# Optimization experiments

Hardware: AMD Instinct MI355X
Metric: run time of the kernel (lower is better)

## Reference

```python
import jax, jax.numpy as jnp
import numpy as np

B, C_IN, H_IMG, W_IMG = 64, 384, 32, 32
D, HEADS = 768, 12
HD = D // HEADS
GS = 16            # attention grid = image_size // 2
ET = 1             # extra tokens
N = GS * GS + ET   # 257
MLP_H = 4 * D
EPS = 1e-5


def _rel_index():
    coords = np.stack(np.meshgrid(np.arange(GS), np.arange(GS), indexing='ij'))  # [2,GS,GS]
    cf = coords.reshape(2, -1)                      # [2, GS*GS]
    rel = (cf[:, :, None] - cf[:, None, :]).transpose(1, 2, 0)  # [P,P,2]
    rel[:, :, 0] += GS - 1
    rel[:, :, 1] += GS - 1
    rel[:, :, 0] *= 2 * GS - 1
    idx = rel.sum(-1)                               # [P,P]
    out = np.zeros((N, N), dtype=np.int32)          # F.pad with zeros for extra tokens
    out[ET:, ET:] = idx
    return out

REL_IDX = jnp.asarray(_rel_index())


def _ln(x, g, b):
    m = x.mean(-1, keepdims=True)
    v = ((x - m) ** 2).mean(-1, keepdims=True)
    return (x - m) / jnp.sqrt(v + EPS) * g + b


def setup_inputs() -> dict:
    key = jax.random.key(0)
    ks = jax.random.split(key, 16)
    s = 0.02
    return {
        "x": jax.random.normal(ks[0], (B, C_IN, H_IMG, W_IMG), jnp.float32),
        "H": 32,
        "W": 32,
        "geo_bias": jax.random.normal(ks[1], (1, N, D), jnp.float32),
        "extra_token": jax.random.normal(ks[2], (1, ET, D), jnp.float32) * s,
        "conv_w": jax.random.normal(ks[3], (D, C_IN, 3, 3), jnp.float32) * np.sqrt(2.0 / (9 * D)),
        "conv_b": jnp.zeros((D,), jnp.float32),
        "pe_g": jnp.ones((D,), jnp.float32),
        "pe_b": jnp.zeros((D,), jnp.float32),
        "n1_g": jnp.ones((D,), jnp.float32),
        "n1_b": jnp.zeros((D,), jnp.float32),
        "qkv_w": jax.random.normal(ks[4], (3 * D, D), jnp.float32) * s,
        "rpb_table": jax.random.normal(ks[5], ((2 * GS - 1) * (2 * GS - 1), HEADS), jnp.float32) * s,
        "proj_w": jax.random.normal(ks[6], (D, D), jnp.float32) * s,
        "proj_b": jnp.zeros((D,), jnp.float32),
        "n2_g": jnp.ones((D,), jnp.float32),
        "n2_b": jnp.zeros((D,), jnp.float32),
        "fc1_w": jax.random.normal(ks[7], (MLP_H, D), jnp.float32) * s,
        "fc1_b": jnp.zeros((MLP_H,), jnp.float32),
        "fc2_w": jax.random.normal(ks[8], (D, MLP_H), jnp.float32) * s,
        "fc2_b": jnp.zeros((D,), jnp.float32),
    }


def reference(x, H, W, geo_bias, extra_token, conv_w, conv_b, pe_g, pe_b,
              n1_g, n1_b, qkv_w, rpb_table, proj_w, proj_b, n2_g, n2_b,
              fc1_w, fc1_b, fc2_w, fc2_b):
    # OverlapPatchEmbed: conv k3 s2 p1 -> [B, D, GS, GS]
    y = jax.lax.conv_general_dilated(x, conv_w, (2, 2), ((1, 1), (1, 1)),
                                     dimension_numbers=('NCHW', 'OIHW', 'NCHW'))
    y = y + conv_b[None, :, None, None]
    y = y.reshape(B, D, GS * GS).transpose(0, 2, 1)   # [B, P, D]
    y = _ln(y, pe_g, pe_b)
    tok = jnp.broadcast_to(extra_token, (B, ET, D))
    y = jnp.concatenate([tok, y], axis=1) + geo_bias  # [B, N, D]

    # Relative attention
    h = _ln(y, n1_g, n1_b)
    qkv = (h @ qkv_w.T).reshape(B, N, 3, HEADS, HD).transpose(2, 0, 3, 1, 4)
    q, k, v = qkv[0] * (HD ** -0.5), qkv[1], qkv[2]   # [B, h, N, d]
    attn = jnp.einsum('bhnd,bhmd->bhnm', q, k)
    bias = rpb_table[REL_IDX].transpose(2, 0, 1)      # [heads, N, N]
    attn = jax.nn.softmax(attn + bias[None], axis=-1)
    o = jnp.einsum('bhnm,bhmd->bhnd', attn, v).transpose(0, 2, 1, 3).reshape(B, N, D)
    y = y + (o @ proj_w.T + proj_b)

    # MLP
    h2 = _ln(y, n2_g, n2_b)
    h2 = jax.nn.gelu(h2 @ fc1_w.T + fc1_b, approximate=False)
    y = y + (h2 @ fc2_w.T + fc2_b)
    return y
```

## Files before the change

kernel.cpp:

```cpp
#include <hip/hip_runtime.h>
#include <hip/hip_bf16.h>
#include <cstdint>

using bf16 = __hip_bfloat16;
typedef __attribute__((ext_vector_type(8))) short short8;
typedef __attribute__((ext_vector_type(4))) float f32x4;


__device__ __forceinline__ void gld_lds16(const bf16* g, bf16* l) {
  __builtin_amdgcn_global_load_lds(
      (const __attribute__((address_space(1))) void*)g,
      (__attribute__((address_space(3))) void*)l, 16, 0, 0);
}

__device__ __forceinline__ unsigned short f2bf_bits(float f) {
  uint32_t u = __builtin_bit_cast(uint32_t, f);
  uint32_t r = (u + 0x7fffu + ((u >> 16) & 1u)) >> 16;
  return (unsigned short)r;
}

__device__ __forceinline__ int xcd_swz(int bid, int nwg) {
  const int q = nwg >> 3, r = nwg & 7;
  const int x = bid & 7, o = bid >> 3;
  return (x < r ? x * (q + 1) : r * (q + 1) + (x - r) * q) + o;
}

__global__ void castf2b(const float* __restrict__ in, bf16* __restrict__ out, int n) {
  int i = blockIdx.x * blockDim.x + threadIdx.x;
  int st = gridDim.x * blockDim.x;
  for (; i < n; i += st) out[i] = __float2bfloat16(in[i]);
}

__global__ void zero_b(bf16* __restrict__ p, int n) {
  int i = blockIdx.x * blockDim.x + threadIdx.x;
  if (i < n) p[i] = __float2bfloat16(0.f);
}

__global__ void convw_reorder(const float* __restrict__ w, bf16* __restrict__ o) {
  int i = blockIdx.x * blockDim.x + threadIdx.x;
  if (i >= 768 * 3456) return;
  int n = i / 3456, r = i % 3456;
  int tap = r / 384, c = r % 384;
  o[i] = __float2bfloat16(w[(long)n * 3456 + c * 9 + tap]);
}

__global__ __launch_bounds__(256, 4)
void nhwc_kernel(const float* __restrict__ x, bf16* __restrict__ xp) {
  __shared__ bf16 T[384 * 33];
  const int biy = blockIdx.x;
  const int b = biy >> 5, iy = biy & 31;
  const int tid = threadIdx.x;
  const int ix = tid & 31, cp = tid >> 5;
  const long xrow = (long)b * 384 * 1024 + iy * 32 + ix;
#pragma unroll
  for (int t = 0; t < 48; ++t) {
    const int c = t * 8 + cp;
    T[c * 33 + ix] = __float2bfloat16(x[xrow + (long)c * 1024]);
  }
  __syncthreads();
  bf16* dst = xp + (((long)b * 34 + iy + 1) * 34 + 1) * 384;
  for (int e4 = tid; e4 < 3072; e4 += 256) {
    const int e = e4 * 4;
    const int ixr = e / 384, c = e % 384;
    ushort4 v;
    v.x = ((const unsigned short*)T)[(c + 0) * 33 + ixr];
    v.y = ((const unsigned short*)T)[(c + 1) * 33 + ixr];
    v.z = ((const unsigned short*)T)[(c + 2) * 33 + ixr];
    v.w = ((const unsigned short*)T)[(c + 3) * 33 + ixr];
    *(ushort4*)(dst + e) = v;
  }
}

template <int EPI>
__global__ __launch_bounds__(256, 2)
void gemm_bt(const bf16* __restrict__ A, const bf16* __restrict__ Bw,
             const float* __restrict__ bias, float* __restrict__ outf,
             bf16* __restrict__ outb, int N, int K, int Mreal, int ntn)
{
  __shared__ bf16 As[2][128 * 64];
  __shared__ bf16 Bs[2][128 * 64];
  const int bid = xcd_swz(blockIdx.x, gridDim.x);
  const int mt = bid / ntn, nt = bid % ntn;
  const int tid = threadIdx.x;
  const int lane = tid & 63, wave = tid >> 6;
  const int wm = wave >> 1, wn = wave & 1;
  const int lr = lane & 15, lg = lane >> 4;

  f32x4 acc[4][4];
#pragma unroll
  for (int i = 0; i < 4; ++i)
#pragma unroll
    for (int j = 0; j < 4; ++j) acc[i][j] = (f32x4){0.f, 0.f, 0.f, 0.f};

  const int arow = tid >> 3;
  const int scol = (((tid & 7) ^ (arow & 7))) * 8;
  const bf16* ag = A + ((long)mt * 128 + arow) * K + scol;
  const bf16* bg = Bw + ((long)nt * 128 + arow) * K + scol;

  const int xs0 = ((lg)     ^ (lr & 7)) * 16;
  const int xs1 = ((lg + 4) ^ (lr & 7)) * 16;
  const char* pa0 = (const char*)(&As[0][0]) + (wm * 64 + lr) * 128 + xs0;
  const char* pa1 = (const char*)(&As[0][0]) + (wm * 64 + lr) * 128 + xs1;
  const char* pb0 = (const char*)(&Bs[0][0]) + (wn * 64 + lr) * 128 + xs0;
  const char* pb1 = (const char*)(&Bs[0][0]) + (wn * 64 + lr) * 128 + xs1;

  auto stage = [&](int kt, int buf) {
    const int k0 = kt << 6;
#pragma unroll
    for (int j = 0; j < 4; ++j) {
      gld_lds16(ag + (long)(j * 32) * K + k0, &As[buf][(j * 256 + tid) * 8]);
      gld_lds16(bg + (long)(j * 32) * K + k0, &Bs[buf][(j * 256 + tid) * 8]);
    }
  };
  auto compute = [&](int buf) {
    const int bo = buf * 16384;
#pragma unroll
    for (int ks = 0; ks < 2; ++ks) {
      const char* pa = ks ? pa1 : pa0;
      const char* pb = ks ? pb1 : pb0;
      short8 af[4], bv[4];
#pragma unroll
      for (int i = 0; i < 4; ++i) af[i] = *(const short8*)(pa + bo + i * 2048);
#pragma unroll
      for (int i = 0; i < 4; ++i) bv[i] = *(const short8*)(pb + bo + i * 2048);
#pragma unroll
      for (int i = 0; i < 4; ++i)
#pragma unroll
        for (int j = 0; j < 4; ++j)
          acc[i][j] = __builtin_amdgcn_mfma_f32_16x16x32_bf16(af[i], bv[j], acc[i][j], 0, 0, 0);
    }
  };

  const int nk = K >> 6;
  stage(0, 0);
  __syncthreads();
  for (int t = 0; t < nk; t += 2) {
    if (t + 1 < nk) stage(t + 1, 1);
    compute(0);
    __syncthreads();
    if (t + 1 >= nk) break;
    if (t + 2 < nk) stage(t + 2, 0);
    compute(1);
    __syncthreads();
  }

  const int rbase = mt * 128 + wm * 64 + (lane >> 4) * 4;
  const int cbase = nt * 128 + wn * 64 + lr;
#pragma unroll
  for (int i = 0; i < 4; ++i) {
#pragma unroll
    for (int j = 0; j < 4; ++j) {
      const int col = cbase + j * 16;
      float bvv = 0.f;
      if constexpr (EPI != 0) bvv = bias[col];
#pragma unroll
      for (int r = 0; r < 4; ++r) {
        const int row = rbase + i * 16 + r;
        const float v = acc[i][j][r];
        if constexpr (EPI == 0) {
          outb[(long)row * N + col] = __float2bfloat16(v);
        } else if constexpr (EPI == 1) {
          outb[(long)row * N + col] = __float2bfloat16(v + bvv);
        } else if constexpr (EPI == 2) {
          const float t = v + bvv;
          outb[(long)row * N + col] =
              __float2bfloat16(0.5f * t * (1.0f + erff(t * 0.70710678118f)));
        } else {
          if (row < Mreal) {
            const long o = (long)row * N + col;
            outf[o] = outf[o] + v + bvv;
          }
        }
      }
    }
  }
}

__global__ __launch_bounds__(256, 2)
void conv_gemm(const bf16* __restrict__ xp, const bf16* __restrict__ Bw,
               const float* __restrict__ bias, bf16* __restrict__ outb)
{
  __shared__ bf16 As[2][128 * 64];
  __shared__ bf16 Bs[2][128 * 64];
  const int bid = xcd_swz(blockIdx.x, gridDim.x);
  const int mt = bid / 6, nt = bid % 6;
  const int tid = threadIdx.x;
  const int lane = tid & 63, wave = tid >> 6;
  const int wm = wave >> 1, wn = wave & 1;
  const int lr = lane & 15, lg = lane >> 4;

  f32x4 acc[4][4];
#pragma unroll
  for (int i = 0; i < 4; ++i)
#pragma unroll
    for (int j = 0; j < 4; ++j) acc[i][j] = (f32x4){0.f, 0.f, 0.f, 0.f};

  const int arow = tid >> 3;
  const int scol = (((tid & 7) ^ (arow & 7))) * 8;
  long abase[4];
#pragma unroll
  for (int j = 0; j < 4; ++j) {
    const int m = mt * 128 + j * 32 + arow;
    const int b = m >> 8, p = m & 255;
    const int gy = p >> 4, gx = p & 15;
    abase[j] = (((long)b * 34 + 2 * gy) * 34 + 2 * gx) * 384 + scol;
  }
  const bf16* bg = Bw + ((long)nt * 128 + arow) * 3456 + scol;

  const int xs0 = ((lg)     ^ (lr & 7)) * 16;
  const int xs1 = ((lg + 4) ^ (lr & 7)) * 16;
  const char* pa0 = (const char*)(&As[0][0]) + (wm * 64 + lr) * 128 + xs0;
  const char* pa1 = (const char*)(&As[0][0]) + (wm * 64 + lr) * 128 + xs1;
  const char* pb0 = (const char*)(&Bs[0][0]) + (wn * 64 + lr) * 128 + xs0;
  const char* pb1 = (const char*)(&Bs[0][0]) + (wn * 64 + lr) * 128 + xs1;

  auto stage = [&](int kidx, int buf) {
    const int tap = kidx / 6, kc = (kidx % 6) * 64;
    const int toff = ((tap / 3) * 34 + (tap % 3)) * 384 + kc;
#pragma unroll
    for (int j = 0; j < 4; ++j) {
      gld_lds16(xp + abase[j] + toff, &As[buf][(j * 256 + tid) * 8]);
      gld_lds16(bg + (long)(j * 32) * 3456 + kidx * 64, &Bs[buf][(j * 256 + tid) * 8]);
    }
  };
  auto compute = [&](int buf) {
    const int bo = buf * 16384;
#pragma unroll
    for (int ks = 0; ks < 2; ++ks) {
      const char* pa = ks ? pa1 : pa0;
      const char* pb = ks ? pb1 : pb0;
      short8 af[4], bv[4];
#pragma unroll
      for (int i = 0; i < 4; ++i) af[i] = *(const short8*)(pa + bo + i * 2048);
#pragma unroll
      for (int i = 0; i < 4; ++i) bv[i] = *(const short8*)(pb + bo + i * 2048);
#pragma unroll
      for (int i = 0; i < 4; ++i)
#pragma unroll
        for (int j = 0; j < 4; ++j)
          acc[i][j] = __builtin_amdgcn_mfma_f32_16x16x32_bf16(af[i], bv[j], acc[i][j], 0, 0, 0);
    }
  };

  stage(0, 0);
  __syncthreads();
  for (int t = 0; t < 54; t += 2) {
    if (t + 1 < 54) stage(t + 1, 1);
    compute(0);
    __syncthreads();
    if (t + 2 < 54) stage(t + 2, 0);
    compute(1);
    __syncthreads();
  }

  const int rbase = mt * 128 + wm * 64 + (lane >> 4) * 4;
  const int cbase = nt * 128 + wn * 64 + lr;
#pragma unroll
  for (int i = 0; i < 4; ++i) {
#pragma unroll
    for (int j = 0; j < 4; ++j) {
      const int col = cbase + j * 16;
      const float bvv = bias[col];
#pragma unroll
      for (int r = 0; r < 4; ++r) {
        const int row = rbase + i * 16 + r;
        outb[(long)row * 768 + col] = __float2bfloat16(acc[i][j][r] + bvv);
      }
    }
  }
}

__global__ __launch_bounds__(256, 4)
void embed_ln_kernel(const bf16* __restrict__ CO, const float* __restrict__ extra,
                     const float* __restrict__ geo, const float* __restrict__ pe_g,
                     const float* __restrict__ pe_b, const float* __restrict__ n1_g,
                     const float* __restrict__ n1_b, float* __restrict__ y,
                     bf16* __restrict__ H)
{
  const int row = blockIdx.x;
  const int tid = threadIdx.x;
  __shared__ float red[2][4];
  const int wave = tid >> 6, lane = tid & 63;
  if (row >= 16448) {
#pragma unroll
    for (int u = 0; u < 3; ++u) H[(long)row * 768 + tid + u * 256] = __float2bfloat16(0.f);
    return;
  }
  const int b = row / 257, t = row % 257;
  float yv[3];
  if (t == 0) {
#pragma unroll
    for (int u = 0; u < 3; ++u) {
      const int d = tid + u * 256;
      yv[u] = extra[d] + geo[d];
    }
  } else {
    const bf16* src = CO + (long)(b * 256 + (t - 1)) * 768;
    float v[3]; float s = 0.f, s2 = 0.f;
#pragma unroll
    for (int u = 0; u < 3; ++u) {
      v[u] = __bfloat162float(src[tid + u * 256]);
      s += v[u]; s2 += v[u] * v[u];
    }
#pragma unroll
    for (int off = 32; off > 0; off >>= 1) { s += __shfl_xor(s, off); s2 += __shfl_xor(s2, off); }
    if (lane == 0) { red[0][wave] = s; red[1][wave] = s2; }
    __syncthreads();
    const float S = red[0][0] + red[0][1] + red[0][2] + red[0][3];
    const float S2 = red[1][0] + red[1][1] + red[1][2] + red[1][3];
    const float mean = S * (1.f / 768.f);
    const float var = S2 * (1.f / 768.f) - mean * mean;
    const float rinv = rsqrtf(var + 1e-5f);
    __syncthreads();
#pragma unroll
    for (int u = 0; u < 3; ++u) {
      const int d = tid + u * 256;
      yv[u] = (v[u] - mean) * rinv * pe_g[d] + pe_b[d] + geo[(long)t * 768 + d];
    }
  }
#pragma unroll
  for (int u = 0; u < 3; ++u) y[(long)row * 768 + tid + u * 256] = yv[u];
  float s = 0.f, s2 = 0.f;
#pragma unroll
  for (int u = 0; u < 3; ++u) { s += yv[u]; s2 += yv[u] * yv[u]; }
#pragma unroll
  for (int off = 32; off > 0; off >>= 1) { s += __shfl_xor(s, off); s2 += __shfl_xor(s2, off); }
  if (lane == 0) { red[0][wave] = s; red[1][wave] = s2; }
  __syncthreads();
  const float S = red[0][0] + red[0][1] + red[0][2] + red[0][3];
  const float S2 = red[1][0] + red[1][1] + red[1][2] + red[1][3];
  const float mean = S * (1.f / 768.f);
  const float var = S2 * (1.f / 768.f) - mean * mean;
  const float rinv = rsqrtf(var + 1e-5f);
#pragma unroll
  for (int u = 0; u < 3; ++u) {
    const int d = tid + u * 256;
    H[(long)row * 768 + d] = __float2bfloat16((yv[u] - mean) * rinv * n1_g[d] + n1_b[d]);
  }
}

__global__ __launch_bounds__(256, 4)
void ln_kernel(const float* __restrict__ y, const float* __restrict__ g,
               const float* __restrict__ bta, bf16* __restrict__ H, int Mreal)
{
  const int row = blockIdx.x;
  const int tid = threadIdx.x;
  if (row >= Mreal) {
#pragma unroll
    for (int u = 0; u < 3; ++u) H[(long)row * 768 + tid + u * 256] = __float2bfloat16(0.f);
    return;
  }
  const float* src = y + (long)row * 768;
  float v[3]; float s = 0.f, s2 = 0.f;
#pragma unroll
  for (int u = 0; u < 3; ++u) { v[u] = src[tid + u * 256]; s += v[u]; s2 += v[u] * v[u]; }
#pragma unroll
  for (int off = 32; off > 0; off >>= 1) { s += __shfl_xor(s, off); s2 += __shfl_xor(s2, off); }
  __shared__ float red[2][4];
  const int wave = tid >> 6, lane = tid & 63;
  if (lane == 0) { red[0][wave] = s; red[1][wave] = s2; }
  __syncthreads();
  const float S = red[0][0] + red[0][1] + red[0][2] + red[0][3];
  const float S2 = red[1][0] + red[1][1] + red[1][2] + red[1][3];
  const float mean = S * (1.f / 768.f);
  const float var = S2 * (1.f / 768.f) - mean * mean;
  const float rinv = rsqrtf(var + 1e-5f);
#pragma unroll
  for (int u = 0; u < 3; ++u) {
    const int d = tid + u * 256;
    H[(long)row * 768 + d] = __float2bfloat16((v[u] - mean) * rinv * g[d] + bta[d]);
  }
}

__global__ void rpbT_kernel(const float* __restrict__ rpb, float* __restrict__ rpbT) {
  int i = blockIdx.x * blockDim.x + threadIdx.x;
  if (i >= 12 * 961) return;
  int h = i / 961, t = i % 961;
  rpbT[i] = rpb[t * 12 + h];
}

__global__ __launch_bounds__(256, 2)
void vtrans_kernel(const bf16* __restrict__ qkv, bf16* __restrict__ vt) {
  __shared__ bf16 Vl[257 * 65];
  const int bh = blockIdx.x;
  const int b = bh / 12, h = bh % 12;
  const long src = (long)b * 257 * 2304 + 1536 + h * 64;
  for (int e = threadIdx.x; e < 257 * 64; e += 256) {
    const int t = e >> 6, d = e & 63;
    Vl[t * 65 + d] = qkv[src + (long)t * 2304 + d];
  }
  __syncthreads();
  const bf16 z = __float2bfloat16(0.f);
  const long dst = (long)bh * 64 * 320;
  for (int e = threadIdx.x; e < 64 * 320; e += 256) {
    const int d = e / 320, tp = e % 320;
    vt[dst + e] = (tp < 257) ? Vl[tp * 65 + d] : z;
  }
}

__global__ __launch_bounds__(256, 2)
void attn_mfma(const bf16* __restrict__ qkv, const bf16* __restrict__ vt,
               const float* __restrict__ rpbT, bf16* __restrict__ O)
{
  __shared__ bf16 Ks[64 * 64];
  __shared__ bf16 Vts[64 * 64];
  __shared__ float rpb_s[961];
  __shared__ bf16 Pl[4][16 * 72];

  const int bid = blockIdx.x;
  const int qb = bid % 5;
  const int bh = bid / 5;
  const int h = bh % 12, b = bh / 12;
  const int tid = threadIdx.x;
  const int lane = tid & 63, w = tid >> 6;
  const int lr = lane & 15, g = lane >> 4;

  for (int t = tid; t < 961; t += 256) rpb_s[t] = rpbT[h * 961 + t];

  const long qkv_bh = (long)b * 257 * 2304 + h * 64;
  const long vt_bh = (long)bh * 64 * 320;

  const int q_tok = qb * 64 + w * 16 + lr;
  const bf16* qp = qkv + qkv_bh + (long)q_tok * 2304;
  short8 qf[2];
  qf[0] = *(const short8*)(qp + g * 8);
  qf[1] = *(const short8*)(qp + 32 + g * 8);

  f32x4 ao[4];
#pragma unroll
  for (int df = 0; df < 4; ++df) ao[df] = (f32x4){0.f, 0.f, 0.f, 0.f};
  float mval = -1e30f, l = 0.f;

  for (int ck = 0; ck < 5; ++ck) {
    const int c0 = ck * 64;
#pragma unroll
    for (int it = 0; it < 2; ++it) {
      const int beta = it * 256 + tid;
      const int row = beta >> 3, cb = beta & 7;
      const int cbs = cb ^ (row & 7);
      gld_lds16(qkv + qkv_bh + (long)(c0 + row) * 2304 + 768 + cbs * 8, &Ks[beta * 8]);
      gld_lds16(vt + vt_bh + (long)row * 320 + c0 + cbs * 8, &Vts[beta * 8]);
    }
    __syncthreads();

    f32x4 st[4];
#pragma unroll
    for (int kf = 0; kf < 4; ++kf) st[kf] = (f32x4){0.f, 0.f, 0.f, 0.f};
#pragma unroll
    for (int ks = 0; ks < 2; ++ks) {
#pragma unroll
      for (int kf = 0; kf < 4; ++kf) {
        const int row = kf * 16 + lr;
        const short8 kfrag = *(const short8*)&Ks[row * 64 + ((ks * 4 + g) ^ (row & 7)) * 8];
        st[kf] = __builtin_amdgcn_mfma_f32_16x16x32_bf16(kfrag, qf[ks], st[kf], 0, 0, 0);
      }
    }

    float p[4][4];
    float t = -1e30f;
#pragma unroll
    for (int kf = 0; kf < 4; ++kf) {
#pragma unroll
      for (int r = 0; r < 4; ++r) {
        const int key = c0 + kf * 16 + g * 4 + r;
        float s;
        if (key < 257) {
          int idx = 0;
          if (q_tok > 0 && key > 0) {
            const int qi = q_tok - 1, kj = key - 1;
            idx = ((qi >> 4) - (kj >> 4) + 15) * 31 + ((qi & 15) - (kj & 15) + 15);
            idx = idx < 0 ? 0 : (idx > 960 ? 960 : idx);
          }
          s = 0.125f * st[kf][r] + rpb_s[idx];
        } else {
          s = -1e30f;
        }
        p[kf][r] = s;
        t = fmaxf(t, s);
      }
    }
    t = fmaxf(t, __shfl_xor(t, 16));
    t = fmaxf(t, __shfl_xor(t, 32));
    const float mnew = fmaxf(mval, t);
    const float corr = __expf(mval - mnew);
    mval = mnew;
    float ps = 0.f;
#pragma unroll
    for (int kf = 0; kf < 4; ++kf)
#pragma unroll
      for (int r = 0; r < 4; ++r) { p[kf][r] = __expf(p[kf][r] - mnew); ps += p[kf][r]; }
    ps += __shfl_xor(ps, 16);
    ps += __shfl_xor(ps, 32);
    l = l * corr + ps;

#pragma unroll
    for (int r = 0; r < 4; ++r) {
      const float cr = __shfl(corr, g * 4 + r);
#pragma unroll
      for (int df = 0; df < 4; ++df) ao[df][r] *= cr;
    }

    bf16* plw = &Pl[w][0];
#pragma unroll
    for (int kf = 0; kf < 4; ++kf) {
      uint2 pw;
      pw.x = ((uint32_t)f2bf_bits(p[kf][1]) << 16) | (uint32_t)f2bf_bits(p[kf][0]);
      pw.y = ((uint32_t)f2bf_bits(p[kf][3]) << 16) | (uint32_t)f2bf_bits(p[kf][2]);
      *(uint2*)&plw[lr * 72 + kf * 16 + g * 4] = pw;
    }

#pragma unroll
    for (int ks = 0; ks < 2; ++ks) {
      const short8 pa = *(const short8*)&plw[lr * 72 + ks * 32 + g * 8];
#pragma unroll
      for (int df = 0; df < 4; ++df) {
        const int row = df * 16 + lr;
        const short8 vfrag = *(const short8*)&Vts[row * 64 + ((ks * 4 + g) ^ (row & 7)) * 8];
        ao[df] = __builtin_amdgcn_mfma_f32_16x16x32_bf16(pa, vfrag, ao[df], 0, 0, 0);
      }
    }
    __syncthreads();
  }

  const float rl = 1.0f / l;
#pragma unroll
  for (int r = 0; r < 4; ++r) {
    const float rr = __shfl(rl, g * 4 + r);
    const int qg = qb * 64 + w * 16 + g * 4 + r;
    if (qg < 257) {
      bf16* op = O + ((long)b * 257 + qg) * 768 + h * 64;
#pragma unroll
      for (int df = 0; df < 4; ++df)
        op[df * 16 + lr] = __float2bfloat16(ao[df][r] * rr);
    }
  }
}


extern "C" void kernel_launch(void* const* d_in, const int* in_sizes, int n_in,
                              void* d_out, int out_size, void* d_ws, size_t ws_size,
                              hipStream_t stream) {
  (void)in_sizes; (void)n_in; (void)out_size;
  const float* x      = (const float*)d_in[0];
  const float* geo    = (const float*)d_in[3];
  const float* extra  = (const float*)d_in[4];
  const float* conv_w = (const float*)d_in[5];
  const float* conv_b = (const float*)d_in[6];
  const float* pe_g   = (const float*)d_in[7];
  const float* pe_b   = (const float*)d_in[8];
  const float* n1_g   = (const float*)d_in[9];
  const float* n1_b   = (const float*)d_in[10];
  const float* qkv_w  = (const float*)d_in[11];
  const float* rpb    = (const float*)d_in[12];
  const float* proj_w = (const float*)d_in[13];
  const float* proj_b = (const float*)d_in[14];
  const float* n2_g   = (const float*)d_in[15];
  const float* n2_b   = (const float*)d_in[16];
  const float* fc1_w  = (const float*)d_in[17];
  const float* fc1_b  = (const float*)d_in[18];
  const float* fc2_w  = (const float*)d_in[19];
  const float* fc2_b  = (const float*)d_in[20];
  float* out = (float*)d_out;

  constexpr size_t SZ_WCONV = 768UL * 3456 * 2;
  constexpr size_t SZ_WQKV  = 2304UL * 768 * 2;
  constexpr size_t SZ_WPROJ = 768UL * 768 * 2;
  constexpr size_t SZ_WFC1  = 3072UL * 768 * 2;
  constexpr size_t SZ_WFC2  = 768UL * 3072 * 2;
  constexpr size_t SZ_H     = 16512UL * 768 * 2;
  constexpr size_t SZ_A     = 16384UL * 3456 * 2;
  constexpr size_t SZ_B     = 16512UL * 768 * 2;
  constexpr size_t TOTAL = SZ_WCONV + SZ_WQKV + SZ_WPROJ + SZ_WFC1 + SZ_WFC2 + SZ_H + SZ_A + SZ_B;
  if (ws_size < TOTAL) return;

  char* ws = (char*)d_ws;
  bf16* Wconv = (bf16*)ws;                    ws += SZ_WCONV;
  bf16* Wqkv  = (bf16*)ws;                    ws += SZ_WQKV;
  bf16* Wproj = (bf16*)ws;                    ws += SZ_WPROJ;
  bf16* Wfc1  = (bf16*)ws;                    ws += SZ_WFC1;
  bf16* Wfc2  = (bf16*)ws;                    ws += SZ_WFC2;
  bf16* Hb    = (bf16*)ws;                    ws += SZ_H;
  char* regA  = ws;                           ws += SZ_A;
  char* regB  = ws;
  bf16* XP   = (bf16*)regA;
  bf16* QKV  = (bf16*)regA;
  bf16* MLPH = (bf16*)regA;
  constexpr size_t SZ_QKV = 16512UL * 2304 * 2;
  constexpr size_t SZ_XP  = 64UL * 34 * 34 * 384 * 2;
  bf16* Vt   = (bf16*)(regA + SZ_QKV);
  bf16* CO   = (bf16*)regB;
  bf16* Oat  = (bf16*)regB;
  float* rpbTp = (float*)Hb;

  convw_reorder<<<10368, 256, 0, stream>>>(conv_w, Wconv);
  castf2b<<<2048, 256, 0, stream>>>(qkv_w,  Wqkv, 1769472);
  castf2b<<<1024, 256, 0, stream>>>(proj_w, Wproj, 589824);
  castf2b<<<2048, 256, 0, stream>>>(fc1_w,  Wfc1, 2359296);
  castf2b<<<2048, 256, 0, stream>>>(fc2_w,  Wfc2, 2359296);
  hipMemsetAsync(XP, 0, SZ_XP, stream);
  nhwc_kernel<<<2048, 256, 0, stream>>>(x, XP);
  conv_gemm<<<128 * 6, 256, 0, stream>>>(XP, Wconv, conv_b, CO);
  embed_ln_kernel<<<16512, 256, 0, stream>>>(CO, extra, geo, pe_g, pe_b, n1_g, n1_b, out, Hb);
  gemm_bt<0><<<129 * 18, 256, 0, stream>>>(Hb, Wqkv, nullptr, nullptr, QKV, 2304, 768, 16448, 18);
  rpbT_kernel<<<46, 256, 0, stream>>>(rpb, rpbTp);
  vtrans_kernel<<<768, 256, 0, stream>>>(QKV, Vt);
  zero_b<<<192, 256, 0, stream>>>(Oat + 16448L * 768, 49152);
  attn_mfma<<<3840, 256, 0, stream>>>(QKV, Vt, rpbTp, Oat);
  gemm_bt<3><<<129 * 6, 256, 0, stream>>>(Oat, Wproj, proj_b, out, nullptr, 768, 768, 16448, 6);
  ln_kernel<<<16512, 256, 0, stream>>>(out, n2_g, n2_b, Hb, 16448);
  gemm_bt<2><<<129 * 24, 256, 0, stream>>>(Hb, Wfc1, fc1_b, nullptr, MLPH, 3072, 768, 16448, 24);
  gemm_bt<3><<<129 * 6, 256, 0, stream>>>(MLPH, Wfc2, fc2_b, out, nullptr, 768, 3072, 16448, 6);
}
```

Baseline: 712.1 us.

## Replace double-buffered LDS staging with single-buffer load-sync-compute loop in GEMMs

Both the generic GEMM and the conv implicit-GEMM drop their two-stage LDS ping-pong and use one buffer per operand, with a load, barrier, compute, barrier sequence each K step. This halves LDS use per block (32KB to 16KB), which could allow more resident blocks per CU. The cost is losing the overlap of global-to-LDS loads with MFMA compute inside a block, so latency has to be hidden by other resident waves instead.

```diff
diff --git a/kernel.cpp b/kernel.cpp
--- a/kernel.cpp
+++ b/kernel.cpp
@@ -77,8 +77,8 @@
              const float* __restrict__ bias, float* __restrict__ outf,
              bf16* __restrict__ outb, int N, int K, int Mreal, int ntn)
 {
-  __shared__ bf16 As[2][128 * 64];
-  __shared__ bf16 Bs[2][128 * 64];
+  __shared__ bf16 As[128 * 64];
+  __shared__ bf16 Bs[128 * 64];
   const int bid = xcd_swz(blockIdx.x, gridDim.x);
   const int mt = bid / ntn, nt = bid % ntn;
   const int tid = threadIdx.x;
@@ -99,48 +99,35 @@
 
   const int xs0 = ((lg)     ^ (lr & 7)) * 16;
   const int xs1 = ((lg + 4) ^ (lr & 7)) * 16;
-  const char* pa0 = (const char*)(&As[0][0]) + (wm * 64 + lr) * 128 + xs0;
-  const char* pa1 = (const char*)(&As[0][0]) + (wm * 64 + lr) * 128 + xs1;
-  const char* pb0 = (const char*)(&Bs[0][0]) + (wn * 64 + lr) * 128 + xs0;
-  const char* pb1 = (const char*)(&Bs[0][0]) + (wn * 64 + lr) * 128 + xs1;
-
-  auto stage = [&](int kt, int buf) {
-    const int k0 = kt << 6;
+  const char* pa0 = (const char*)(&As[0]) + (wm * 64 + lr) * 128 + xs0;
+  const char* pa1 = (const char*)(&As[0]) + (wm * 64 + lr) * 128 + xs1;
+  const char* pb0 = (const char*)(&Bs[0]) + (wn * 64 + lr) * 128 + xs0;
+  const char* pb1 = (const char*)(&Bs[0]) + (wn * 64 + lr) * 128 + xs1;
+
+  const int nk = K >> 6;
+  for (int t = 0; t < nk; ++t) {
+    const int k0 = t << 6;
 #pragma unroll
     for (int j = 0; j < 4; ++j) {
-      gld_lds16(ag + (long)(j * 32) * K + k0, &As[buf][(j * 256 + tid) * 8]);
-      gld_lds16(bg + (long)(j * 32) * K + k0, &Bs[buf][(j * 256 + tid) * 8]);
-    }
-  };
-  auto compute = [&](int buf) {
-    const int bo = buf * 16384;
+      gld_lds16(ag + (long)(j * 32) * K + k0, &As[(j * 256 + tid) * 8]);
+      gld_lds16(bg + (long)(j * 32) * K + k0, &Bs[(j * 256 + tid) * 8]);
+    }
+    __syncthreads();
 #pragma unroll
     for (int ks = 0; ks < 2; ++ks) {
       const char* pa = ks ? pa1 : pa0;
       const char* pb = ks ? pb1 : pb0;
       short8 af[4], bv[4];
 #pragma unroll
-      for (int i = 0; i < 4; ++i) af[i] = *(const short8*)(pa + bo + i * 2048);
-#pragma unroll
-      for (int i = 0; i < 4; ++i) bv[i] = *(const short8*)(pb + bo + i * 2048);
+      for (int i = 0; i < 4; ++i) af[i] = *(const short8*)(pa + i * 2048);
+#pragma unroll
+      for (int i = 0; i < 4; ++i) bv[i] = *(const short8*)(pb + i * 2048);
 #pragma unroll
       for (int i = 0; i < 4; ++i)
 #pragma unroll
         for (int j = 0; j < 4; ++j)
           acc[i][j] = __builtin_amdgcn_mfma_f32_16x16x32_bf16(af[i], bv[j], acc[i][j], 0, 0, 0);
     }
-  };
-
-  const int nk = K >> 6;
-  stage(0, 0);
-  __syncthreads();
-  for (int t = 0; t < nk; t += 2) {
-    if (t + 1 < nk) stage(t + 1, 1);
-    compute(0);
-    __syncthreads();
-    if (t + 1 >= nk) break;
-    if (t + 2 < nk) stage(t + 2, 0);
-    compute(1);
     __syncthreads();
   }
 
@@ -180,8 +167,8 @@
 void conv_gemm(const bf16* __restrict__ xp, const bf16* __restrict__ Bw,
                const float* __restrict__ bias, bf16* __restrict__ outb)
 {
-  __shared__ bf16 As[2][128 * 64];
-  __shared__ bf16 Bs[2][128 * 64];
+  __shared__ bf16 As[128 * 64];
+  __shared__ bf16 Bs[128 * 64];
   const int bid = xcd_swz(blockIdx.x, gridDim.x);
   const int mt = bid / 6, nt = bid % 6;
   const int tid = threadIdx.x;
@@ -209,47 +196,35 @@
 
   const int xs0 = ((lg)     ^ (lr & 7)) * 16;
   const int xs1 = ((lg + 4) ^ (lr & 7)) * 16;
-  const char* pa0 = (const char*)(&As[0][0]) + (wm * 64 + lr) * 128 + xs0;
-  const char* pa1 = (const char*)(&As[0][0]) + (wm * 64 + lr) * 128 + xs1;
-  const char* pb0 = (const char*)(&Bs[0][0]) + (wn * 64 + lr) * 128 + xs0;
-  const char* pb1 = (const char*)(&Bs[0][0]) + (wn * 64 + lr) * 128 + xs1;
-
-  auto stage = [&](int kidx, int buf) {
-    const int tap = kidx / 6, kc = (kidx % 6) * 64;
+  const char* pa0 = (const char*)(&As[0]) + (wm * 64 + lr) * 128 + xs0;
+  const char* pa1 = (const char*)(&As[0]) + (wm * 64 + lr) * 128 + xs1;
+  const char* pb0 = (const char*)(&Bs[0]) + (wn * 64 + lr) * 128 + xs0;
+  const char* pb1 = (const char*)(&Bs[0]) + (wn * 64 + lr) * 128 + xs1;
+
+  for (int t = 0; t < 54; ++t) {
+    const int tap = t / 6, kc = (t % 6) * 64;
     const int toff = ((tap / 3) * 34 + (tap % 3)) * 384 + kc;
 #pragma unroll
     for (int j = 0; j < 4; ++j) {
-      gld_lds16(xp + abase[j] + toff, &As[buf][(j * 256 + tid) * 8]);
-      gld_lds16(bg + (long)(j * 32) * 3456 + kidx * 64, &Bs[buf][(j * 256 + tid) * 8]);
-    }
-  };
-  auto compute = [&](int buf) {
-    const int bo = buf * 16384;
+      gld_lds16(xp + abase[j] + toff, &As[(j * 256 + tid) * 8]);
+      gld_lds16(bg + (long)(j * 32) * 3456 + t * 64, &Bs[(j * 256 + tid) * 8]);
+    }
+    __syncthreads();
 #pragma unroll
     for (int ks = 0; ks < 2; ++ks) {
       const char* pa = ks ? pa1 : pa0;
       const char* pb = ks ? pb1 : pb0;
       short8 af[4], bv[4];
 #pragma unroll
-      for (int i = 0; i < 4; ++i) af[i] = *(const short8*)(pa + bo + i * 2048);
-#pragma unroll
-      for (int i = 0; i < 4; ++i) bv[i] = *(const short8*)(pb + bo + i * 2048);
+      for (int i = 0; i < 4; ++i) af[i] = *(const short8*)(pa + i * 2048);
+#pragma unroll
+      for (int i = 0; i < 4; ++i) bv[i] = *(const short8*)(pb + i * 2048);
 #pragma unroll
       for (int i = 0; i < 4; ++i)
 #pragma unroll
         for (int j = 0; j < 4; ++j)
           acc[i][j] = __builtin_amdgcn_mfma_f32_16x16x32_bf16(af[i], bv[j], acc[i][j], 0, 0, 0);
     }
-  };
-
-  stage(0, 0);
-  __syncthreads();
-  for (int t = 0; t < 54; t += 2) {
-    if (t + 1 < 54) stage(t + 1, 1);
-    compute(0);
-    __syncthreads();
-    if (t + 2 < 54) stage(t + 2, 0);
-    compute(1);
     __syncthreads();
   }
 
```

Measured after the change: 615.2 us. 1.16x faster.
